# Performance work log

Hardware: AMD Instinct MI355X
Metric: run time of the kernel (lower is better)

The kernel has to match this reference:

```python
import jax, jax.numpy as jnp
import numpy as np

EMB = 1024
HEADS = 16
HEAD_DIM = EMB // HEADS


def setup_inputs() -> dict:
    key = jax.random.key(0)
    ks = jax.random.split(key, 6)
    B, S = 4, 1024
    inputs = jax.random.normal(ks[0], (B, S, EMB), dtype=jnp.float32)
    # causal mask: 1.0 where attention is disallowed (added * -1e9 in the layer)
    mask = (1.0 - jnp.tril(jnp.ones((S, S), dtype=jnp.float32)))[None, None, :, :]
    scale = 1.0 / np.sqrt(EMB)
    wq = jax.random.normal(ks[1], (EMB, EMB), dtype=jnp.float32) * scale
    wk = jax.random.normal(ks[2], (EMB, EMB), dtype=jnp.float32) * scale
    wv = jax.random.normal(ks[3], (EMB, EMB), dtype=jnp.float32) * scale
    wo = jax.random.normal(ks[4], (EMB, EMB), dtype=jnp.float32) * scale
    zb = jnp.zeros((EMB,), dtype=jnp.float32)
    return {"inputs": inputs, "mask": mask, "wq": wq, "bq": zb, "wk": wk,
            "bk": zb, "wv": wv, "bv": zb, "wo": wo, "bo": zb}


def _split_heads(t, B):
    # [B, S, E] -> [B, H, S, Dh]
    return t.reshape(B, -1, HEADS, HEAD_DIM).transpose(0, 2, 1, 3)


def reference(inputs, mask, wq, bq, wk, bk, wv, bv, wo, bo):
    B = inputs.shape[0]
    q = _split_heads(inputs @ wq + bq, B)
    k = _split_heads(inputs @ wk + bk, B)
    v = _split_heads(inputs @ wv + bv, B)
    # NOTE: source divides by sqrt(sqrt(head_num)) = head_num**0.25
    scores = jnp.einsum('bhsd,bhtd->bhst', q, k) / jnp.asarray(HEADS, inputs.dtype) ** 0.25
    if mask is not None:
        scores = scores + mask * -1e9
    attn = jax.nn.softmax(scores, axis=-1)
    z = jnp.einsum('bhst,bhtd->bhsd', attn, v)
    # Faithful to source: reshape [B,H,S,Dh] -> [B,S,E] WITHOUT transposing heads back
    z = z.reshape(B, -1, EMB)
    return z @ wo + bo
```

## Files before the change

kernel.cpp:

```cpp
#include <hip/hip_runtime.h>
#include <hip/hip_bf16.h>
#include <stdint.h>

typedef __attribute__((ext_vector_type(8))) short short8;
typedef __attribute__((ext_vector_type(4))) float float4v;

#define SEQ   1024
#define NQKV  3072

__device__ __forceinline__ float bf2f(ushort h) {
    union { uint u; float f; } c; c.u = ((uint)h) << 16; return c.f;
}
__device__ __forceinline__ ushort f2bf(float f) {
    union { uint u; float f; } c; c.f = f;
    uint u = c.u;
    return (ushort)((u + 0x7fffu + ((u >> 16) & 1u)) >> 16);
}
__device__ __forceinline__ void gl2lds16(const ushort* g, ushort* l) {
    __builtin_amdgcn_global_load_lds(
        (const __attribute__((address_space(1))) unsigned int*)(g),
        (__attribute__((address_space(3))) unsigned int*)(l),
        16, 0, 0);
}

__global__ void detect_k(const uint* __restrict__ x, int* __restrict__ flag) {
    __shared__ int cnt[256];
    int h = 0;
    for (int i = threadIdx.x; i < 4096; i += 256) {
        uint w = x[i];
        uint e = (w >> 7) & 0xFFu;
        h += (e >= 100u && e <= 130u) ? 1 : 0;
    }
    cnt[threadIdx.x] = h;
    __syncthreads();
    if (threadIdx.x == 0) {
        int s = 0;
        for (int i = 0; i < 256; i++) s += cnt[i];
        flag[0] = (s > 2048) ? 0 : 1;
    }
}

__global__ __launch_bounds__(256) void xcvt_k(const void* __restrict__ x,
                                              ushort* __restrict__ xc,
                                              const int* __restrict__ flag) {
    if (!*flag) return;
    int i = (blockIdx.x * 256 + threadIdx.x) * 4;
    const float* xf = (const float*)x;
    float4 v = *(const float4*)(xf + i);
    ushort4 o;
    o.x = f2bf(v.x); o.y = f2bf(v.y); o.z = f2bf(v.z); o.w = f2bf(v.w);
    *(ushort4*)(xc + i) = o;
}

__global__ void biascat_k(const void* __restrict__ bq, const void* __restrict__ bk,
                          const void* __restrict__ bv, const void* __restrict__ bo,
                          const int* __restrict__ flag, ushort* __restrict__ bout) {
    int i = blockIdx.x * 256 + threadIdx.x;
    int sel = i >> 10, j = i & 1023;
    const void* p = (sel == 0) ? bq : (sel == 1) ? bk : (sel == 2) ? bv : bo;
    bout[i] = (*flag) ? f2bf(((const float*)p)[j]) : ((const ushort*)p)[j];
}

__global__ __launch_bounds__(256) void transpose4_k(const void* __restrict__ w0,
                                                    const void* __restrict__ w1,
                                                    const void* __restrict__ w2,
                                                    const void* __restrict__ w3,
                                                    ushort* __restrict__ outall,
                                                    const int* __restrict__ flag) {
    __shared__ ushort tile[64][72];
    int z = blockIdx.z;
    const void* in = (z == 0) ? w0 : (z == 1) ? w1 : (z == 2) ? w2 : w3;
    ushort* out = outall + (size_t)z * 1024 * 1024;
    int k0 = blockIdx.x * 64;
    int n0 = blockIdx.y * 64;
    int t = threadIdx.x;
    int r = t >> 3, c = (t & 7) * 8;
    bool isf = (*flag != 0);
#pragma unroll
    for (int p = 0; p < 2; p++) {
        int rr = r + p * 32;
        if (isf) {
            const float* src = (const float*)in + (size_t)(k0 + rr) * 1024 + n0 + c;
            float4 v0 = *(const float4*)src;
            float4 v1 = *(const float4*)(src + 4);
            tile[rr][c + 0] = f2bf(v0.x); tile[rr][c + 1] = f2bf(v0.y);
            tile[rr][c + 2] = f2bf(v0.z); tile[rr][c + 3] = f2bf(v0.w);
            tile[rr][c + 4] = f2bf(v1.x); tile[rr][c + 5] = f2bf(v1.y);
            tile[rr][c + 6] = f2bf(v1.z); tile[rr][c + 7] = f2bf(v1.w);
        } else {
            uint4 v = *(const uint4*)((const ushort*)in + (size_t)(k0 + rr) * 1024 + n0 + c);
            *(uint4*)&tile[rr][c] = v;
        }
    }
    __syncthreads();
#pragma unroll
    for (int p = 0; p < 2; p++) {
        int n = r + p * 32;
        ushort vals[8];
#pragma unroll
        for (int j = 0; j < 8; j++) vals[j] = tile[c + j][n];
        *(uint4*)(out + (size_t)(n0 + n) * 1024 + k0 + c) = *(uint4*)vals;
    }
}

__global__ __launch_bounds__(256) void vtrans_k(const ushort* __restrict__ qkv,
                                                ushort* __restrict__ vt) {
    __shared__ ushort tile[64][72];
    int t0 = blockIdx.x * 64;
    int bh = blockIdx.y;
    int b = bh >> 4, h = bh & 15;
    int t = threadIdx.x;
    int r = t >> 3, c = (t & 7) * 8;
#pragma unroll
    for (int p = 0; p < 2; p++) {
        int rr = r + p * 32;
        uint4 v = *(const uint4*)(qkv + (size_t)(b * 1024 + t0 + rr) * NQKV + 2048 + h * 64 + c);
        *(uint4*)&tile[rr][c] = v;
    }
    __syncthreads();
#pragma unroll
    for (int p = 0; p < 2; p++) {
        int d = r + p * 32;
        ushort vals[8];
#pragma unroll
        for (int j = 0; j < 8; j++) vals[j] = tile[c + j][d];
        *(uint4*)(vt + ((size_t)bh * 64 + d) * 1024 + t0 + c) = *(uint4*)vals;
    }
}

template <int BM, bool DUAL>
__global__ __launch_bounds__(256) void gemm_k(const ushort* __restrict__ Araw,
                                              const ushort* __restrict__ Aconv,
                                              const ushort* __restrict__ BT,
                                              const ushort* __restrict__ bias,
                                              void* __restrict__ C,
                                              const int* __restrict__ flag,
                                              int M, int N, int K) {
    constexpr int RM = BM / 32;
    __shared__ ushort As[BM * 32];
    __shared__ ushort Bs[128 * 32];
    int n0 = blockIdx.x * 128, m0 = blockIdx.y * BM;
    int t = threadIdx.x;
    int w = t >> 6, lane = t & 63, q = lane >> 4, ln = lane & 15;
    int wr = w >> 1, wc = w & 1;
    const ushort* A = (*flag) ? Aconv : Araw;

    float4v acc[RM][4];
#pragma unroll
    for (int r = 0; r < RM; r++)
#pragma unroll
        for (int cc = 0; cc < 4; cc++) acc[r][cc] = (float4v){0.f, 0.f, 0.f, 0.f};

    for (int k0 = 0; k0 < K; k0 += 32) {
#pragma unroll
        for (int j = 0; j < BM / 64; j++) {
            int c = j * 256 + t;
            int row = c >> 2, s = c & 3;
            int kc = s ^ ((row >> 1) & 3);
            gl2lds16(A + (size_t)(m0 + row) * K + k0 + kc * 8, &As[c * 8]);
        }
#pragma unroll
        for (int j = 0; j < 2; j++) {
            int c = j * 256 + t;
            int row = c >> 2, s = c & 3;
            int kc = s ^ ((row >> 1) & 3);
            gl2lds16(BT + (size_t)(n0 + row) * K + k0 + kc * 8, &Bs[c * 8]);
        }
        __syncthreads();
        short8 af[RM], bf[4];
#pragma unroll
        for (int r = 0; r < RM; r++) {
            int row = wr * (BM / 2) + r * 16 + ln;
            af[r] = *(const short8*)&As[((row << 2) | (q ^ ((row >> 1) & 3))) * 8];
        }
#pragma unroll
        for (int cc = 0; cc < 4; cc++) {
            int col = wc * 64 + cc * 16 + ln;
            bf[cc] = *(const short8*)&Bs[((col << 2) | (q ^ ((col >> 1) & 3))) * 8];
        }
#pragma unroll
        for (int r = 0; r < RM; r++)
#pragma unroll
            for (int cc = 0; cc < 4; cc++)
                acc[r][cc] = __builtin_amdgcn_mfma_f32_16x16x32_bf16(af[r], bf[cc], acc[r][cc], 0, 0, 0);
        __syncthreads();
    }

    bool outf = DUAL && (*flag != 0);
#pragma unroll
    for (int cc = 0; cc < 4; cc++) {
        int n = n0 + wc * 64 + cc * 16 + ln;
        float bs = bf2f(bias[n]);
#pragma unroll
        for (int r = 0; r < RM; r++) {
#pragma unroll
            for (int i = 0; i < 4; i++) {
                int m = m0 + wr * (BM / 2) + r * 16 + q * 4 + i;
                float v = acc[r][cc][i] + bs;
                if (outf) ((float*)C)[(size_t)m * N + n] = v;
                else      ((ushort*)C)[(size_t)m * N + n] = f2bf(v);
            }
        }
    }
}

__global__ __launch_bounds__(256) void attn_k(const ushort* __restrict__ qkv,
                                              const ushort* __restrict__ vt,
                                              ushort* __restrict__ zp) {
    __shared__ ushort Ks[2][64 * 64];
    __shared__ ushort Vs[2][64 * 64];
    __shared__ ushort PA[4][16 * 76];
    __shared__ ushort PB[4][16 * 76];
    int pr = blockIdx.x;
    int bh = blockIdx.y;
    int b = bh >> 4, h = bh & 15;
    int t = threadIdx.x;
    int w = t >> 6, lane = t & 63, q = lane >> 4, ln = lane & 15;

    const float CE = 0.72134752f;

    const ushort* Qp = qkv + (size_t)(b * SEQ) * NQKV + h * 64;
    const ushort* Kp = qkv + (size_t)(b * SEQ) * NQKV + 1024 + h * 64;
    const ushort* Vt = vt + (size_t)bh * 64 * 1024;

    int c0 = t, c1 = 256 + t;
    int row0 = c0 >> 3, kc0 = (c0 & 7) ^ (row0 & 7);
    int row1 = c1 >> 3, kc1 = (c1 & 7) ^ (row1 & 7);

    int tiA = pr, tiB = 15 - pr;
    int swA = tiA * 64 + w * 16, swB = tiB * 64 + w * 16;

    short8 aqA0 = *(const short8*)(Qp + (size_t)(swA + ln) * NQKV + q * 8);
    short8 aqA1 = *(const short8*)(Qp + (size_t)(swA + ln) * NQKV + 32 + q * 8);
    short8 aqB0 = *(const short8*)(Qp + (size_t)(swB + ln) * NQKV + q * 8);
    short8 aqB1 = *(const short8*)(Qp + (size_t)(swB + ln) * NQKV + 32 + q * 8);

    float lA[4], lB[4];
    float4v oA[4], oB[4];
#pragma unroll
    for (int i = 0; i < 4; i++) { lA[i] = 0.f; lB[i] = 0.f; }
#pragma unroll
    for (int nb = 0; nb < 4; nb++) {
        oA[nb] = (float4v){0.f, 0.f, 0.f, 0.f};
        oB[nb] = (float4v){0.f, 0.f, 0.f, 0.f};
    }

    gl2lds16(Kp + (size_t)row0 * NQKV + kc0 * 8, &Ks[0][c0 * 8]);
    gl2lds16(Vt + (size_t)row0 * 1024 + kc0 * 8, &Vs[0][c0 * 8]);
    gl2lds16(Kp + (size_t)row1 * NQKV + kc1 * 8, &Ks[0][c1 * 8]);
    gl2lds16(Vt + (size_t)row1 * 1024 + kc1 * 8, &Vs[0][c1 * 8]);

    auto tile_step = [&](int cur, int t0, int sw, short8 aq0, short8 aq1,
                         float* lp, float4v* o, ushort* Pw, bool maskdiag) {
        float4v s[4];
#pragma unroll
        for (int nb = 0; nb < 4; nb++) {
            int row = nb * 16 + ln;
            short8 kf0 = *(const short8*)&Ks[cur][((row << 3) | (q ^ (row & 7))) * 8];
            short8 kf1 = *(const short8*)&Ks[cur][((row << 3) | ((4 + q) ^ (row & 7))) * 8];
            s[nb] = (float4v){0.f, 0.f, 0.f, 0.f};
            s[nb] = __builtin_amdgcn_mfma_f32_16x16x32_bf16(aq0, kf0, s[nb], 0, 0, 0);
            s[nb] = __builtin_amdgcn_mfma_f32_16x16x32_bf16(aq1, kf1, s[nb], 0, 0, 0);
        }
        float p[4][4];
        if (!maskdiag) {
#pragma unroll
            for (int nb = 0; nb < 4; nb++)
#pragma unroll
                for (int i = 0; i < 4; i++) p[nb][i] = exp2f(s[nb][i] * CE);
        } else {
#pragma unroll
            for (int nb = 0; nb < 4; nb++)
#pragma unroll
                for (int i = 0; i < 4; i++) {
                    int srow = sw + q * 4 + i;
                    int col = t0 + nb * 16 + ln;
                    p[nb][i] = exp2f((col <= srow) ? s[nb][i] * CE : -1e30f);
                }
        }
#pragma unroll
        for (int i = 0; i < 4; i++)
            lp[i] += (p[0][i] + p[1][i]) + (p[2][i] + p[3][i]);
#pragma unroll
        for (int nb = 0; nb < 4; nb++)
#pragma unroll
            for (int i = 0; i < 4; i++)
                Pw[(q * 4 + i) * 76 + nb * 16 + ln] = f2bf(p[nb][i]);
        asm volatile("s_waitcnt lgkmcnt(0)\n" ::: "memory");
        short8 ap0 = *(const short8*)&Pw[ln * 76 + q * 8];
        short8 ap1 = *(const short8*)&Pw[ln * 76 + 32 + q * 8];
#pragma unroll
        for (int nb = 0; nb < 4; nb++) {
            int row = nb * 16 + ln;
            short8 bv0 = *(const short8*)&Vs[cur][((row << 3) | (q ^ (row & 7))) * 8];
            short8 bv1 = *(const short8*)&Vs[cur][((row << 3) | ((4 + q) ^ (row & 7))) * 8];
            o[nb] = __builtin_amdgcn_mfma_f32_16x16x32_bf16(ap0, bv0, o[nb], 0, 0, 0);
            o[nb] = __builtin_amdgcn_mfma_f32_16x16x32_bf16(ap1, bv1, o[nb], 0, 0, 0);
        }
    };

    for (int kt = 0; kt <= tiB; kt++) {
        int cur = kt & 1;
        int t0 = kt * 64;
        __syncthreads();
        if (kt < tiB) {
            int nt0 = t0 + 64, nxt = cur ^ 1;
            gl2lds16(Kp + (size_t)(nt0 + row0) * NQKV + kc0 * 8, &Ks[nxt][c0 * 8]);
            gl2lds16(Vt + (size_t)row0 * 1024 + nt0 + kc0 * 8, &Vs[nxt][c0 * 8]);
            gl2lds16(Kp + (size_t)(nt0 + row1) * NQKV + kc1 * 8, &Ks[nxt][c1 * 8]);
            gl2lds16(Vt + (size_t)row1 * 1024 + nt0 + kc1 * 8, &Vs[nxt][c1 * 8]);
        }
        tile_step(cur, t0, swB, aqB0, aqB1, lB, oB, PB[w], kt == tiB);
        if (kt <= tiA)
            tile_step(cur, t0, swA, aqA0, aqA1, lA, oA, PA[w], kt == tiA);
    }

#pragma unroll
    for (int i = 0; i < 4; i++) {
        float sA = lA[i], sB = lB[i];
#pragma unroll
        for (int mk = 1; mk < 16; mk <<= 1) {
            sA += __shfl_xor(sA, mk, 64);
            sB += __shfl_xor(sB, mk, 64);
        }
        lA[i] = sA; lB[i] = sB;
    }
#pragma unroll
    for (int nb = 0; nb < 4; nb++) {
#pragma unroll
        for (int i = 0; i < 4; i++) {
            int d = nb * 16 + ln;
            int srowA = swA + q * 4 + i;
            int spA = h * 64 + (srowA >> 4);
            int epA = ((srowA & 15) << 6) + d;
            zp[((size_t)(b * SEQ + spA)) * 1024 + epA] = f2bf(oA[nb][i] / lA[i]);
            int srowB = swB + q * 4 + i;
            int spB = h * 64 + (srowB >> 4);
            int epB = ((srowB & 15) << 6) + d;
            zp[((size_t)(b * SEQ + spB)) * 1024 + epB] = f2bf(oB[nb][i] / lB[i]);
        }
    }
}

extern "C" void kernel_launch(void* const* d_in, const int* in_sizes, int n_in,
                              void* d_out, int out_size, void* d_ws, size_t ws_size,
                              hipStream_t stream) {
    const void* X  = d_in[0];
    const void* wq = d_in[2];
    const void* bq = d_in[3];
    const void* wk = d_in[4];
    const void* bk = d_in[5];
    const void* wv = d_in[6];
    const void* bv = d_in[7];
    const void* wo = d_in[8];
    const void* bo = d_in[9];

    char* ws = (char*)d_ws;
    int*    flag  = (int*)ws;
    ushort* biasq = (ushort*)(ws + 4096);
    ushort* WTall = (ushort*)(ws + 12288);
    ushort* Xc    = (ushort*)(ws + 8400896);
    ushort* QKV   = (ushort*)(ws + 16789504);
    ushort* VT    = (ushort*)(ws + 41955328);
    ushort* WTo   = WTall + 3 * 1024 * 1024;
    ushort* ZP    = Xc;

    detect_k<<<1, 256, 0, stream>>>((const uint*)X, flag);
    xcvt_k<<<4096, 256, 0, stream>>>(X, Xc, flag);
    biascat_k<<<16, 256, 0, stream>>>(bq, bk, bv, bo, flag, biasq);
    transpose4_k<<<dim3(16, 16, 4), 256, 0, stream>>>(wq, wk, wv, wo, WTall, flag);
    gemm_k<128, false><<<dim3(24, 32), 256, 0, stream>>>(
        (const ushort*)X, Xc, WTall, biasq, QKV, flag, 4096, NQKV, 1024);
    vtrans_k<<<dim3(16, 64), 256, 0, stream>>>(QKV, VT);
    attn_k<<<dim3(8, 64), 256, 0, stream>>>(QKV, VT, ZP);
    gemm_k<64, true><<<dim3(8, 64), 256, 0, stream>>>(
        ZP, ZP, WTo, biasq + 3072, d_out, flag, 4096, 1024, 1024);
}
```

Measured before the change: 202.0 us.

## Split paired causal query tiles across two wave groups in 512-thread attention blocks

The attention kernel now runs 512 threads per block. Two groups of four waves each own one of the paired query tiles (pr and 15-pr), where before each wave processed both tiles one after the other. The K/V tile loads are shared by the doubled thread count, so each thread issues one load per buffer instead of two. The aim is more parallelism and latency hiding per block. The cost is idle waves in the short-tile group once it passes its diagonal, while they still take part in every __syncthreads.

Result: no change. 199.3 us (-1.3%).

```diff
diff --git a/kernel.cpp b/kernel.cpp
--- a/kernel.cpp
+++ b/kernel.cpp
@@ -204,18 +204,19 @@
     }
 }
 
-__global__ __launch_bounds__(256) void attn_k(const ushort* __restrict__ qkv,
+__global__ __launch_bounds__(512) void attn_k(const ushort* __restrict__ qkv,
                                               const ushort* __restrict__ vt,
                                               ushort* __restrict__ zp) {
     __shared__ ushort Ks[2][64 * 64];
     __shared__ ushort Vs[2][64 * 64];
-    __shared__ ushort PA[4][16 * 76];
-    __shared__ ushort PB[4][16 * 76];
+    __shared__ ushort P[8][16 * 76];
     int pr = blockIdx.x;
     int bh = blockIdx.y;
     int b = bh >> 4, h = bh & 15;
     int t = threadIdx.x;
-    int w = t >> 6, lane = t & 63, q = lane >> 4, ln = lane & 15;
+    int w = t >> 6;
+    int grp = w >> 2;
+    int lane = t & 63, q = lane >> 4, ln = lane & 15;
 
     const float CE = 0.72134752f;
 
@@ -223,81 +224,24 @@
     const ushort* Kp = qkv + (size_t)(b * SEQ) * NQKV + 1024 + h * 64;
     const ushort* Vt = vt + (size_t)bh * 64 * 1024;
 
-    int c0 = t, c1 = 256 + t;
-    int row0 = c0 >> 3, kc0 = (c0 & 7) ^ (row0 & 7);
-    int row1 = c1 >> 3, kc1 = (c1 & 7) ^ (row1 & 7);
-
-    int tiA = pr, tiB = 15 - pr;
-    int swA = tiA * 64 + w * 16, swB = tiB * 64 + w * 16;
-
-    short8 aqA0 = *(const short8*)(Qp + (size_t)(swA + ln) * NQKV + q * 8);
-    short8 aqA1 = *(const short8*)(Qp + (size_t)(swA + ln) * NQKV + 32 + q * 8);
-    short8 aqB0 = *(const short8*)(Qp + (size_t)(swB + ln) * NQKV + q * 8);
-    short8 aqB1 = *(const short8*)(Qp + (size_t)(swB + ln) * NQKV + 32 + q * 8);
-
-    float lA[4], lB[4];
-    float4v oA[4], oB[4];
-#pragma unroll
-    for (int i = 0; i < 4; i++) { lA[i] = 0.f; lB[i] = 0.f; }
-#pragma unroll
-    for (int nb = 0; nb < 4; nb++) {
-        oA[nb] = (float4v){0.f, 0.f, 0.f, 0.f};
-        oB[nb] = (float4v){0.f, 0.f, 0.f, 0.f};
-    }
-
-    gl2lds16(Kp + (size_t)row0 * NQKV + kc0 * 8, &Ks[0][c0 * 8]);
-    gl2lds16(Vt + (size_t)row0 * 1024 + kc0 * 8, &Vs[0][c0 * 8]);
-    gl2lds16(Kp + (size_t)row1 * NQKV + kc1 * 8, &Ks[0][c1 * 8]);
-    gl2lds16(Vt + (size_t)row1 * 1024 + kc1 * 8, &Vs[0][c1 * 8]);
-
-    auto tile_step = [&](int cur, int t0, int sw, short8 aq0, short8 aq1,
-                         float* lp, float4v* o, ushort* Pw, bool maskdiag) {
-        float4v s[4];
-#pragma unroll
-        for (int nb = 0; nb < 4; nb++) {
-            int row = nb * 16 + ln;
-            short8 kf0 = *(const short8*)&Ks[cur][((row << 3) | (q ^ (row & 7))) * 8];
-            short8 kf1 = *(const short8*)&Ks[cur][((row << 3) | ((4 + q) ^ (row & 7))) * 8];
-            s[nb] = (float4v){0.f, 0.f, 0.f, 0.f};
-            s[nb] = __builtin_amdgcn_mfma_f32_16x16x32_bf16(aq0, kf0, s[nb], 0, 0, 0);
-            s[nb] = __builtin_amdgcn_mfma_f32_16x16x32_bf16(aq1, kf1, s[nb], 0, 0, 0);
-        }
-        float p[4][4];
-        if (!maskdiag) {
-#pragma unroll
-            for (int nb = 0; nb < 4; nb++)
-#pragma unroll
-                for (int i = 0; i < 4; i++) p[nb][i] = exp2f(s[nb][i] * CE);
-        } else {
-#pragma unroll
-            for (int nb = 0; nb < 4; nb++)
-#pragma unroll
-                for (int i = 0; i < 4; i++) {
-                    int srow = sw + q * 4 + i;
-                    int col = t0 + nb * 16 + ln;
-                    p[nb][i] = exp2f((col <= srow) ? s[nb][i] * CE : -1e30f);
-                }
-        }
-#pragma unroll
-        for (int i = 0; i < 4; i++)
-            lp[i] += (p[0][i] + p[1][i]) + (p[2][i] + p[3][i]);
-#pragma unroll
-        for (int nb = 0; nb < 4; nb++)
-#pragma unroll
-            for (int i = 0; i < 4; i++)
-                Pw[(q * 4 + i) * 76 + nb * 16 + ln] = f2bf(p[nb][i]);
-        asm volatile("s_waitcnt lgkmcnt(0)\n" ::: "memory");
-        short8 ap0 = *(const short8*)&Pw[ln * 76 + q * 8];
-        short8 ap1 = *(const short8*)&Pw[ln * 76 + 32 + q * 8];
-#pragma unroll
-        for (int nb = 0; nb < 4; nb++) {
-            int row = nb * 16 + ln;
-            short8 bv0 = *(const short8*)&Vs[cur][((row << 3) | (q ^ (row & 7))) * 8];
-            short8 bv1 = *(const short8*)&Vs[cur][((row << 3) | ((4 + q) ^ (row & 7))) * 8];
-            o[nb] = __builtin_amdgcn_mfma_f32_16x16x32_bf16(ap0, bv0, o[nb], 0, 0, 0);
-            o[nb] = __builtin_amdgcn_mfma_f32_16x16x32_bf16(ap1, bv1, o[nb], 0, 0, 0);
-        }
-    };
+    int row0 = t >> 3, kc0 = (t & 7) ^ (row0 & 7);
+
+    int tiB = 15 - pr;
+    int ti = grp ? tiB : pr;
+    int sw = ti * 64 + (w & 3) * 16;
+
+    short8 aq0 = *(const short8*)(Qp + (size_t)(sw + ln) * NQKV + q * 8);
+    short8 aq1 = *(const short8*)(Qp + (size_t)(sw + ln) * NQKV + 32 + q * 8);
+
+    float lp[4];
+    float4v o[4];
+#pragma unroll
+    for (int i = 0; i < 4; i++) lp[i] = 0.f;
+#pragma unroll
+    for (int nb = 0; nb < 4; nb++) o[nb] = (float4v){0.f, 0.f, 0.f, 0.f};
+
+    gl2lds16(Kp + (size_t)row0 * NQKV + kc0 * 8, &Ks[0][t * 8]);
+    gl2lds16(Vt + (size_t)row0 * 1024 + kc0 * 8, &Vs[0][t * 8]);
 
     for (int kt = 0; kt <= tiB; kt++) {
         int cur = kt & 1;
@@ -305,39 +249,76 @@
         __syncthreads();
         if (kt < tiB) {
             int nt0 = t0 + 64, nxt = cur ^ 1;
-            gl2lds16(Kp + (size_t)(nt0 + row0) * NQKV + kc0 * 8, &Ks[nxt][c0 * 8]);
-            gl2lds16(Vt + (size_t)row0 * 1024 + nt0 + kc0 * 8, &Vs[nxt][c0 * 8]);
-            gl2lds16(Kp + (size_t)(nt0 + row1) * NQKV + kc1 * 8, &Ks[nxt][c1 * 8]);
-            gl2lds16(Vt + (size_t)row1 * 1024 + nt0 + kc1 * 8, &Vs[nxt][c1 * 8]);
-        }
-        tile_step(cur, t0, swB, aqB0, aqB1, lB, oB, PB[w], kt == tiB);
-        if (kt <= tiA)
-            tile_step(cur, t0, swA, aqA0, aqA1, lA, oA, PA[w], kt == tiA);
-    }
-
+            gl2lds16(Kp + (size_t)(nt0 + row0) * NQKV + kc0 * 8, &Ks[nxt][t * 8]);
+            gl2lds16(Vt + (size_t)row0 * 1024 + nt0 + kc0 * 8, &Vs[nxt][t * 8]);
+        }
+        if (kt <= ti) {
+            float4v s[4];
+#pragma unroll
+            for (int nb = 0; nb < 4; nb++) {
+                int row = nb * 16 + ln;
+                short8 kf0 = *(const short8*)&Ks[cur][((row << 3) | (q ^ (row & 7))) * 8];
+                short8 kf1 = *(const short8*)&Ks[cur][((row << 3) | ((4 + q) ^ (row & 7))) * 8];
+                s[nb] = (float4v){0.f, 0.f, 0.f, 0.f};
+                s[nb] = __builtin_amdgcn_mfma_f32_16x16x32_bf16(aq0, kf0, s[nb], 0, 0, 0);
+                s[nb] = __builtin_amdgcn_mfma_f32_16x16x32_bf16(aq1, kf1, s[nb], 0, 0, 0);
+            }
+            float p[4][4];
+            if (kt < ti) {
+#pragma unroll
+                for (int nb = 0; nb < 4; nb++)
+#pragma unroll
+                    for (int i = 0; i < 4; i++) p[nb][i] = exp2f(s[nb][i] * CE);
+            } else {
+#pragma unroll
+                for (int nb = 0; nb < 4; nb++)
+#pragma unroll
+                    for (int i = 0; i < 4; i++) {
+                        int srow = sw + q * 4 + i;
+                        int col = t0 + nb * 16 + ln;
+                        p[nb][i] = exp2f((col <= srow) ? s[nb][i] * CE : -1e30f);
+                    }
+            }
+#pragma unroll
+            for (int i = 0; i < 4; i++)
+                lp[i] += (p[0][i] + p[1][i]) + (p[2][i] + p[3][i]);
+#pragma unroll
+            for (int nb = 0; nb < 4; nb++)
+#pragma unroll
+                for (int i = 0; i < 4; i++)
+                    P[w][(q * 4 + i) * 76 + nb * 16 + ln] = f2bf(p[nb][i]);
+            asm volatile("s_waitcnt lgkmcnt(0)\n" ::: "memory");
+            short8 ap0 = *(const short8*)&P[w][ln * 76 + q * 8];
+            short8 ap1 = *(const short8*)&P[w][ln * 76 + 32 + q * 8];
+#pragma unroll
+            for (int nb = 0; nb < 4; nb++) {
+                int row = nb * 16 + ln;
+                short8 bv0 = *(const short8*)&Vs[cur][((row << 3) | (q ^ (row & 7))) * 8];
+                short8 bv1 = *(const short8*)&Vs[cur][((row << 3) | ((4 + q) ^ (row & 7))) * 8];
+                o[nb] = __builtin_amdgcn_mfma_f32_16x16x32_bf16(ap0, bv0, o[nb], 0, 0, 0);
+                o[nb] = __builtin_amdgcn_mfma_f32_16x16x32_bf16(ap1, bv1, o[nb], 0, 0, 0);
+            }
+        }
+    }
+
+    float l_i[4];
 #pragma unroll
     for (int i = 0; i < 4; i++) {
-        float sA = lA[i], sB = lB[i];
-#pragma unroll
-        for (int mk = 1; mk < 16; mk <<= 1) {
-            sA += __shfl_xor(sA, mk, 64);
-            sB += __shfl_xor(sB, mk, 64);
-        }
-        lA[i] = sA; lB[i] = sB;
+        float s = lp[i];
+#pragma unroll
+        for (int mk = 1; mk < 16; mk <<= 1) s += __shfl_xor(s, mk, 64);
+        l_i[i] = s;
     }
 #pragma unroll
     for (int nb = 0; nb < 4; nb++) {
 #pragma unroll
         for (int i = 0; i < 4; i++) {
+            int srow = sw + q * 4 + i;
             int d = nb * 16 + ln;
-            int srowA = swA + q * 4 + i;
-            int spA = h * 64 + (srowA >> 4);
-            int epA = ((srowA & 15) << 6) + d;
-            zp[((size_t)(b * SEQ + spA)) * 1024 + epA] = f2bf(oA[nb][i] / lA[i]);
-            int srowB = swB + q * 4 + i;
-            int spB = h * 64 + (srowB >> 4);
-            int epB = ((srowB & 15) << 6) + d;
-            zp[((size_t)(b * SEQ + spB)) * 1024 + epB] = f2bf(oB[nb][i] / lB[i]);
+            float z = o[nb][i] / l_i[i];
+            int sp = h * 64 + (srow >> 4);
+            int ep = ((srow & 15) << 6) + d;
+            zp[((size_t)(b * SEQ + sp)) * 1024 + ep] = f2bf(z);
         }
     }
 }
@@ -372,7 +353,7 @@
     gemm_k<128, false><<<dim3(24, 32), 256, 0, stream>>>(
         (const ushort*)X, Xc, WTall, biasq, QKV, flag, 4096, NQKV, 1024);
     vtrans_k<<<dim3(16, 64), 256, 0, stream>>>(QKV, VT);
-    attn_k<<<dim3(8, 64), 256, 0, stream>>>(QKV, VT, ZP);
+    attn_k<<<dim3(8, 64), 512, 0, stream>>>(QKV, VT, ZP);
     gemm_k<64, true><<<dim3(8, 64), 256, 0, stream>>>(
         ZP, ZP, WTo, biasq + 3072, d_out, flag, 4096, 1024, 1024);
 }
```
